# Kernel tuning notes

Hardware: AMD Instinct MI355X
Metric: run time of the kernel (lower is better)

The kernel has to match this reference:

```python
import jax, jax.numpy as jnp
import numpy as np

EMBED = 1024
HEADS = 16

def setup_inputs() -> dict:
    key = jax.random.key(0)
    k1, k2, k3, k4, k5 = jax.random.split(key, 5)
    x = jax.random.normal(k1, (2, 2048, EMBED), dtype=jnp.float32)
    s = 1.0 / np.sqrt(EMBED)
    W_atten = jax.random.normal(k2, (EMBED, 3 * EMBED), dtype=jnp.float32) * s
    b_atten = jax.random.normal(k3, (3 * EMBED,), dtype=jnp.float32) * 0.01
    W_proj = jax.random.normal(k4, (EMBED, EMBED), dtype=jnp.float32) * s
    b_proj = jax.random.normal(k5, (EMBED,), dtype=jnp.float32) * 0.01
    return {"x": x, "W_atten": W_atten, "b_atten": b_atten, "W_proj": W_proj, "b_proj": b_proj}

def reference(x, W_atten, b_atten, W_proj, b_proj):
    B, T, C = x.shape
    H = HEADS
    hs = C // H
    qkv = x @ W_atten + b_atten  # [B,T,3C]
    # NOTE: original splits as k, q, v (k first)
    k, q, v = jnp.split(qkv, 3, axis=2)
    k = k.reshape(B, T, H, hs).transpose(0, 2, 1, 3)  # [B,H,T,hs]
    q = q.reshape(B, T, H, hs).transpose(0, 2, 1, 3)
    v = v.reshape(B, T, H, hs).transpose(0, 2, 1, 3)
    scores = jnp.einsum('bhqd,bhkd->bhqk', q, k) / jnp.sqrt(jnp.float32(hs))
    causal = jnp.tril(jnp.ones((T, T), dtype=bool))
    scores = jnp.where(causal[None, None, :, :], scores, jnp.float32(-jnp.inf))
    att = jax.nn.softmax(scores, axis=-1)
    out = jnp.einsum('bhqk,bhkd->bhqd', att, v)  # [B,H,T,hs]
    out = out.transpose(0, 2, 1, 3).reshape(B, T, C)
    return out @ W_proj + b_proj
```

## Files before the change

kernel.cpp:

```cpp
#include <hip/hip_runtime.h>

typedef unsigned short u16;
typedef unsigned int u32;
typedef __bf16 bf16;
typedef bf16 bf16x8 __attribute__((ext_vector_type(8)));
typedef float f32x4 __attribute__((ext_vector_type(4)));
typedef u32 u32x4 __attribute__((ext_vector_type(4)));
typedef u16 u16x4 __attribute__((ext_vector_type(4)));

#define EMBED 1024
#define HEADS 16
#define HS 64
#define BATCH 2
#define SEQ 2048
#define M_TOT (BATCH * SEQ)
#define N_QKV (3 * EMBED)
#define KDIM  EMBED

#define CSCALE 0.18033688011112042f
#define MREF (64.0f * CSCALE)

__device__ __forceinline__ u16 f2bf(float f) {
  u32 u = __builtin_bit_cast(u32, f);
  u32 r = u + 0x7fffu + ((u >> 16) & 1u);
  return (u16)(r >> 16);
}
__device__ __forceinline__ float bf2f(u16 h) {
  return __builtin_bit_cast(float, (u32)h << 16);
}
__device__ __forceinline__ bf16x8 frag16(const u16* p) {
  return __builtin_bit_cast(bf16x8, *(const u32x4*)p);
}
__device__ __forceinline__ bf16x8 frag16u(const u32* p) {
  return __builtin_bit_cast(bf16x8, *(const u32x4*)p);
}
__device__ __forceinline__ float cl(float v) {
  return fminf(fmaxf(v, -3.0e4f), 3.0e4f);
}
__device__ __forceinline__ u32 pk2bf(float lo, float hi) {
  const u32 ul = __builtin_bit_cast(u32, lo) + 0x8000u;
  const u32 uh = __builtin_bit_cast(u32, hi) + 0x8000u;
  return (ul >> 16) | (uh & 0xFFFF0000u);
}

typedef __attribute__((address_space(1))) void gvoid;
typedef __attribute__((address_space(3))) void lvoid;
__device__ __forceinline__ void glds16(const u16* g, u16* l) {
  __builtin_amdgcn_global_load_lds((gvoid*)g, (lvoid*)l, 16, 0, 0);
}

__global__ __launch_bounds__(256) void convert_kernel(
    const float* __restrict__ in, u16* __restrict__ out, int n4) {
  const int i = blockIdx.x * 256 + threadIdx.x;
  if (i < n4) {
    f32x4 v = *(const f32x4*)(in + (size_t)i * 4);
    u16x4 pk;
#pragma unroll
    for (int j = 0; j < 4; j++) pk[j] = f2bf(v[j]);
    *(u16x4*)(out + (size_t)i * 4) = pk;
  }
}

__global__ __launch_bounds__(256) void transpose_conv_kernel(
    const float* __restrict__ in, u16* __restrict__ out, int R, int C) {
  __shared__ u16 tile[32][33];
  const int c0 = blockIdx.x * 32;
  const int r0 = blockIdx.y * 32;
  const int tx = threadIdx.x;
  const int ty = threadIdx.y;
#pragma unroll
  for (int i = 0; i < 32; i += 8)
    tile[ty + i][tx] = f2bf(in[(size_t)(r0 + ty + i) * C + c0 + tx]);
  __syncthreads();
#pragma unroll
  for (int i = 0; i < 32; i += 8)
    out[(size_t)(c0 + ty + i) * R + r0 + tx] = tile[tx][ty + i];
}

__global__ __launch_bounds__(256) void gemm_qkv_kernel(
    const u16* __restrict__ A, const u16* __restrict__ wt,
    const u16* __restrict__ bias, u16* __restrict__ kq, u16* __restrict__ vt) {
  __shared__ u16 As[128 * 32];
  __shared__ u16 Bs[128 * 32];
  const int tid = threadIdx.x;
  const int lane = tid & 63;
  const int wave = tid >> 6;
  const int quad = lane >> 4;
  const int l16 = lane & 15;
  const int wr = wave >> 1;
  const int wc = wave & 1;
  const int m0 = blockIdx.y * 128;
  const int n0 = blockIdx.x * 128;

  f32x4 acc[4][4] = {};
  const int grow = tid >> 2;
  const int gcol = (tid & 3) * 8;

  for (int k0 = 0; k0 < KDIM; k0 += 32) {
    __syncthreads();
    glds16(A + (size_t)(m0 + grow) * KDIM + k0 + gcol, As + tid * 8);
    glds16(A + (size_t)(m0 + grow + 64) * KDIM + k0 + gcol, As + 2048 + tid * 8);
    glds16(wt + (size_t)(n0 + grow) * KDIM + k0 + gcol, Bs + tid * 8);
    glds16(wt + (size_t)(n0 + grow + 64) * KDIM + k0 + gcol, Bs + 2048 + tid * 8);
    __syncthreads();

    bf16x8 af[4], bfr[4];
#pragma unroll
    for (int i = 0; i < 4; i++) {
      af[i]  = frag16(As + (wr * 64 + i * 16 + l16) * 32 + quad * 8);
      bfr[i] = frag16(Bs + (wc * 64 + i * 16 + l16) * 32 + quad * 8);
    }
#pragma unroll
    for (int mi = 0; mi < 4; mi++)
#pragma unroll
      for (int ni = 0; ni < 4; ni++)
        acc[mi][ni] = __builtin_amdgcn_mfma_f32_16x16x32_bf16(
            af[mi], bfr[ni], acc[mi][ni], 0, 0, 0);
  }

#pragma unroll
  for (int ni = 0; ni < 4; ni++) {
    const int n = n0 + wc * 64 + ni * 16 + l16;
    const float bv = bf2f(bias[n]);
    if (n < 2 * EMBED) {
#pragma unroll
      for (int mi = 0; mi < 4; mi++)
#pragma unroll
        for (int r = 0; r < 4; r++) {
          const int m = m0 + wr * 64 + mi * 16 + quad * 4 + r;
          kq[(size_t)m * 2048 + n] = f2bf(cl(acc[mi][ni][r] + bv));
        }
    } else {
      const int hd = n - 2 * EMBED;
      const int h2 = hd >> 6;
      const int dc2 = (hd >> 4) & 3;
#pragma unroll
      for (int mi = 0; mi < 4; mi++) {
        const int mbase = m0 + wr * 64 + mi * 16 + quad * 4;
        const int bqi = mbase >> 11;
        const int t0 = mbase & 2047;
        const int kt2 = t0 >> 6;
        const int kc2 = (t0 >> 5) & 1;
        const int qt2 = (t0 >> 3) & 3;
        const int e0 = t0 & 7;
        u16x4 pk;
#pragma unroll
        for (int r = 0; r < 4; r++) pk[r] = f2bf(cl(acc[mi][ni][r] + bv));
        const size_t idx =
            ((((size_t)(bqi * 16 + h2) * 32 + kt2) * 2 + kc2) * 4 + dc2) * 512 +
            (qt2 * 16 + l16) * 8 + e0;
        *(u16x4*)(vt + idx) = pk;
      }
    }
  }
}

__global__ __launch_bounds__(128) void gemm_proj_kernel(
    const u16* __restrict__ A, const u16* __restrict__ wt,
    const u16* __restrict__ bias, float* __restrict__ out) {
  __shared__ u16 As[128 * 32];
  __shared__ u16 Bs[64 * 32];
  const int tid = threadIdx.x;
  const int lane = tid & 63;
  const int wave = tid >> 6;
  const int quad = lane >> 4;
  const int l16 = lane & 15;
  const int m0 = blockIdx.y * 128;
  const int n0 = blockIdx.x * 64;

  f32x4 acc[4][4] = {};
  const int grow = tid >> 2;
  const int gcol = (tid & 3) * 8;

  for (int k0 = 0; k0 < KDIM; k0 += 32) {
    __syncthreads();
#pragma unroll
    for (int p = 0; p < 4; p++)
      glds16(A + (size_t)(m0 + p * 32 + grow) * KDIM + k0 + gcol,
             As + p * 1024 + tid * 8);
#pragma unroll
    for (int p = 0; p < 2; p++)
      glds16(wt + (size_t)(n0 + p * 32 + grow) * KDIM + k0 + gcol,
             Bs + p * 1024 + tid * 8);
    __syncthreads();

    bf16x8 af[4], bfr[4];
#pragma unroll
    for (int i = 0; i < 4; i++) {
      af[i]  = frag16(As + (wave * 64 + i * 16 + l16) * 32 + quad * 8);
      bfr[i] = frag16(Bs + (i * 16 + l16) * 32 + quad * 8);
    }
#pragma unroll
    for (int mi = 0; mi < 4; mi++)
#pragma unroll
      for (int ni = 0; ni < 4; ni++)
        acc[mi][ni] = __builtin_amdgcn_mfma_f32_16x16x32_bf16(
            af[mi], bfr[ni], acc[mi][ni], 0, 0, 0);
  }

#pragma unroll
  for (int ni = 0; ni < 4; ni++) {
    const int n = n0 + ni * 16 + l16;
    const float bv = bf2f(bias[n]);
#pragma unroll
    for (int mi = 0; mi < 4; mi++)
#pragma unroll
      for (int r = 0; r < 4; r++) {
        const int m = m0 + wave * 64 + mi * 16 + quad * 4 + r;
        out[(size_t)m * EMBED + n] = cl(acc[mi][ni][r] + bv);
      }
  }
}

__global__ __launch_bounds__(128) void attn_kernel(
    const u16* __restrict__ kq, const u16* __restrict__ vt,
    u16* __restrict__ att) {
  __shared__ u16 Ks[2][2][64 * 64];

  const int tid = threadIdx.x;
  const int lane = tid & 63;
  const int wave = tid >> 6;
  const int quad = (lane >> 4) & 3;
  const int l16 = lane & 15;
  const bool lohalf = (lane < 32);

  const int bh = blockIdx.x;
  const int yy = (int)blockIdx.y;
  const int qt32 = wave ? yy : (63 - yy);
  const int q0 = qt32 * 32;
  const int bq = bh >> 4;
  const int h = bh & 15;

  int qg[2];
  bf16x8 bq0[2], bq1[2];
#pragma unroll
  for (int g = 0; g < 2; g++) {
    qg[g] = q0 + g * 16 + l16;
    const size_t qrow = (size_t)(bq * SEQ + qg[g]) * 2048 + EMBED + h * HS;
    bq0[g] = frag16(kq + qrow + quad * 8);
    bq1[g] = frag16(kq + qrow + 32 + quad * 8);
  }

  const u16* kb = kq + (size_t)bq * SEQ * 2048 + h * HS;
  const u16* vb2 = vt + (size_t)(bq * 16 + h) * 32 * 4096;

  const int pi = ((l16 >> 2) & 1) * 8 + ((l16 >> 3) & 1) * 2 +
                 ((l16 >> 1) & 1) * 4 + (l16 & 1);
  const int psw = quad ^ (pi & 7);
  const int kap = (quad & 1) * 8 + ((quad >> 1) & 1) * 2;

  u32x4 onesu;
#pragma unroll
  for (int j = 0; j < 4; j++) onesu[j] = 0x3F803F80u;
  const bf16x8 ones8 = __builtin_bit_cast(bf16x8, onesu);

  f32x4 o[2][4] = {};
  f32x4 o4[2] = {};

  const int nkt = (qt32 >> 1) + 1;
  u16* ksw = (u16*)Ks[wave];

#pragma unroll
  for (int p = 0; p < 8; p++) {
    const int row = p * 8 + (lane >> 3);
    const int sgc = (lane & 7) ^ (row & 7);
    glds16(kb + (size_t)row * 2048 + sgc * 8, ksw + row * 64 + (lane & 7) * 8);
  }

  for (int kt = 0; kt < nkt; kt++) {
    const int k0 = kt * 64;
    asm volatile("s_waitcnt vmcnt(0)" ::: "memory");
    if (kt + 1 < nkt) {
      const int kn = k0 + 64;
      u16* dst = ksw + ((kt + 1) & 1) * (64 * 64);
#pragma unroll
      for (int p = 0; p < 8; p++) {
        const int row = p * 8 + (lane >> 3);
        const int sgc = (lane & 7) ^ (row & 7);
        glds16(kb + (size_t)(kn + row) * 2048 + sgc * 8, dst + row * 64 + (lane & 7) * 8);
      }
    }
    const u16* KsB = ksw + (kt & 1) * (64 * 64);

    bf16x8 va[2][4];
#pragma unroll
    for (int kc = 0; kc < 2; kc++)
#pragma unroll
      for (int dc = 0; dc < 4; dc++)
        va[kc][dc] = frag16(vb2 + (size_t)kt * 4096 +
                            ((kc * 4 + dc) * 64 + quad * 16 + l16) * 8);

    f32x4 st[2][4] = {};
    __builtin_amdgcn_s_setprio(1);
#pragma unroll
    for (int sub = 0; sub < 4; sub++) {
      const u16* kr = KsB + (sub * 16 + pi) * 64;
      const bf16x8 ka0 = frag16(kr + psw * 8);
      const bf16x8 ka1 = frag16(kr + (psw ^ 4) * 8);
#pragma unroll
      for (int g = 0; g < 2; g++) {
        st[g][sub] = __builtin_amdgcn_mfma_f32_16x16x32_bf16(
            ka0, bq0[g], st[g][sub], 0, 0, 0);
        st[g][sub] = __builtin_amdgcn_mfma_f32_16x16x32_bf16(
            ka1, bq1[g], st[g][sub], 0, 0, 0);
      }
    }
    __builtin_amdgcn_s_setprio(0);

    const bool diag = (kt == nkt - 1);
#pragma unroll
    for (int g = 0; g < 2; g++) {
      float p[4][4];
      if (diag) {
#pragma unroll
        for (int sub = 0; sub < 4; sub++)
#pragma unroll
          for (int r = 0; r < 4; r++) {
            const int key = k0 + sub * 16 + kap + (r >> 1) * 4 + (r & 1);
            const float e = __builtin_amdgcn_exp2f(st[g][sub][r] * CSCALE - MREF);
            p[sub][r] = (key <= qg[g]) ? e : 0.0f;
          }
      } else {
#pragma unroll
        for (int sub = 0; sub < 4; sub++)
#pragma unroll
          for (int r = 0; r < 4; r++)
            p[sub][r] = __builtin_amdgcn_exp2f(st[g][sub][r] * CSCALE - MREF);
      }

#pragma unroll
      for (int kc = 0; kc < 2; kc++) {
        const int s0 = kc * 2, s1 = kc * 2 + 1;
        const u32 An = pk2bf(p[s0][0], p[s0][1]);
        const u32 Bn = pk2bf(p[s1][0], p[s1][1]);
        const u32 Cn = pk2bf(p[s0][2], p[s0][3]);
        const u32 Dn = pk2bf(p[s1][2], p[s1][3]);
        const u32 V1 = __shfl_xor(lohalf ? Bn : An, 32);
        const u32 V2 = __shfl_xor(lohalf ? Dn : Cn, 32);
        u32x4 pr;
        pr[0] = lohalf ? An : V1;
        pr[1] = lohalf ? V1 : Bn;
        pr[2] = lohalf ? Cn : V2;
        pr[3] = lohalf ? V2 : Dn;
        const bf16x8 pb = __builtin_bit_cast(bf16x8, pr);

        __builtin_amdgcn_s_setprio(1);
#pragma unroll
        for (int dc = 0; dc < 4; dc++)
          o[g][dc] = __builtin_amdgcn_mfma_f32_16x16x32_bf16(
              va[kc][dc], pb, o[g][dc], 0, 0, 0);
        o4[g] = __builtin_amdgcn_mfma_f32_16x16x32_bf16(
            ones8, pb, o4[g], 0, 0, 0);
        __builtin_amdgcn_s_setprio(0);
      }
    }
  }

#pragma unroll
  for (int g = 0; g < 2; g++) {
    const float inv = 1.0f / o4[g][0];
    const size_t obase = (size_t)(bq * SEQ + qg[g]) * EMBED + h * HS;
#pragma unroll
    for (int dc = 0; dc < 4; dc++) {
      u16 sv[4];
#pragma unroll
      for (int r = 0; r < 4; r++) sv[r] = f2bf(cl(o[g][dc][r] * inv));
      *(u32*)(att + obase + dc * 16 + quad * 4) = (u32)sv[0] | ((u32)sv[1] << 16);
      *(u32*)(att + obase + dc * 16 + quad * 4 + 2) = (u32)sv[2] | ((u32)sv[3] << 16);
    }
  }
}

extern "C" void kernel_launch(void* const* d_in, const int* in_sizes, int n_in,
                              void* d_out, int out_size, void* d_ws,
                              size_t ws_size, hipStream_t stream) {
  const float* x       = (const float*)d_in[0];
  const float* W_atten = (const float*)d_in[1];
  const float* b_atten = (const float*)d_in[2];
  const float* W_proj  = (const float*)d_in[3];
  const float* b_proj  = (const float*)d_in[4];

  u16* wt_a = (u16*)d_ws;
  u16* wt_p = wt_a + (size_t)N_QKV * EMBED;
  u16* ba   = wt_p + (size_t)EMBED * EMBED;
  u16* bp   = ba + N_QKV;
  u16* xb   = bp + EMBED;
  u16* kq   = xb + (size_t)M_TOT * KDIM;
  u16* vt   = kq + (size_t)M_TOT * 2048;
  u16* attb = xb;

  convert_kernel<<<(M_TOT * KDIM / 4 + 255) / 256, 256, 0, stream>>>(
      x, xb, M_TOT * KDIM / 4);
  convert_kernel<<<(N_QKV / 4 + 255) / 256, 256, 0, stream>>>(b_atten, ba, N_QKV / 4);
  convert_kernel<<<(EMBED / 4 + 255) / 256, 256, 0, stream>>>(b_proj, bp, EMBED / 4);
  transpose_conv_kernel<<<dim3(N_QKV / 32, EMBED / 32), dim3(32, 8), 0, stream>>>(
      W_atten, wt_a, EMBED, N_QKV);
  transpose_conv_kernel<<<dim3(EMBED / 32, EMBED / 32), dim3(32, 8), 0, stream>>>(
      W_proj, wt_p, EMBED, EMBED);
  gemm_qkv_kernel<<<dim3(N_QKV / 128, M_TOT / 128), 256, 0, stream>>>(
      xb, wt_a, ba, kq, vt);
  attn_kernel<<<dim3(BATCH * HEADS, SEQ / 64), 128, 0, stream>>>(kq, vt, attb);
  gemm_proj_kernel<<<dim3(EMBED / 64, M_TOT / 128), 128, 0, stream>>>(
      attb, wt_p, bp, (float*)d_out);
}
```

Before: 193.3 us.

## Split each attention query tile's key range across two waves and merge via LDS

Previously each 128-thread block gave its two waves different 32-row query tiles, paired to balance causal work. Now both waves share one query tile and each processes half of its key tiles. Wave 1 writes its partial output accumulators and row sums to LDS, and wave 0 adds them before normalizing and storing. The grid's y dimension doubles so all query tiles are still covered. This shortens the per-wave serial loop and raises the number of blocks, at the cost of an LDS reduction, a barrier, and less even work per block since pairs are no longer balanced.

```diff
diff --git a/kernel.cpp b/kernel.cpp
--- a/kernel.cpp
+++ b/kernel.cpp
@@ -225,8 +225,7 @@
   const bool lohalf = (lane < 32);
 
   const int bh = blockIdx.x;
-  const int yy = (int)blockIdx.y;
-  const int qt32 = wave ? yy : (63 - yy);
+  const int qt32 = 63 - (int)blockIdx.y;
   const int q0 = qt32 * 32;
   const int bq = bh >> 4;
   const int h = bh & 15;
@@ -258,21 +257,27 @@
   f32x4 o4[2] = {};
 
   const int nkt = (qt32 >> 1) + 1;
+  const int half = nkt >> 1;
+  const int kstart = wave ? half : 0;
+  const int kend = wave ? nkt : half;
   u16* ksw = (u16*)Ks[wave];
 
-#pragma unroll
-  for (int p = 0; p < 8; p++) {
-    const int row = p * 8 + (lane >> 3);
-    const int sgc = (lane & 7) ^ (row & 7);
-    glds16(kb + (size_t)row * 2048 + sgc * 8, ksw + row * 64 + (lane & 7) * 8);
-  }
-
-  for (int kt = 0; kt < nkt; kt++) {
+  if (kstart < kend) {
+#pragma unroll
+    for (int p = 0; p < 8; p++) {
+      const int row = p * 8 + (lane >> 3);
+      const int sgc = (lane & 7) ^ (row & 7);
+      glds16(kb + (size_t)(kstart * 64 + row) * 2048 + sgc * 8,
+             ksw + (kstart & 1) * 4096 + row * 64 + (lane & 7) * 8);
+    }
+  }
+
+  for (int kt = kstart; kt < kend; kt++) {
     const int k0 = kt * 64;
     asm volatile("s_waitcnt vmcnt(0)" ::: "memory");
-    if (kt + 1 < nkt) {
+    if (kt + 1 < kend) {
       const int kn = k0 + 64;
-      u16* dst = ksw + ((kt + 1) & 1) * (64 * 64);
+      u16* dst = ksw + ((kt + 1) & 1) * 4096;
 #pragma unroll
       for (int p = 0; p < 8; p++) {
         const int row = p * 8 + (lane >> 3);
@@ -280,7 +285,7 @@
         glds16(kb + (size_t)(kn + row) * 2048 + sgc * 8, dst + row * 64 + (lane & 7) * 8);
       }
     }
-    const u16* KsB = ksw + (kt & 1) * (64 * 64);
+    const u16* KsB = ksw + (kt & 1) * 4096;
 
     bf16x8 va[2][4];
 #pragma unroll
@@ -356,17 +361,33 @@
     }
   }
 
-#pragma unroll
-  for (int g = 0; g < 2; g++) {
-    const float inv = 1.0f / o4[g][0];
-    const size_t obase = (size_t)(bq * SEQ + qg[g]) * EMBED + h * HS;
-#pragma unroll
-    for (int dc = 0; dc < 4; dc++) {
-      u16 sv[4];
-#pragma unroll
-      for (int r = 0; r < 4; r++) sv[r] = f2bf(cl(o[g][dc][r] * inv));
-      *(u32*)(att + obase + dc * 16 + quad * 4) = (u32)sv[0] | ((u32)sv[1] << 16);
-      *(u32*)(att + obase + dc * 16 + quad * 4 + 2) = (u32)sv[2] | ((u32)sv[3] << 16);
+  float* cb = (float*)Ks[1];
+  if (wave == 1) {
+#pragma unroll
+    for (int g = 0; g < 2; g++) {
+#pragma unroll
+      for (int dc = 0; dc < 4; dc++)
+        *(f32x4*)(cb + ((g * 4 + dc) * 64 + lane) * 4) = o[g][dc];
+      cb[2048 + g * 64 + lane] = o4[g][0];
+    }
+  }
+  __syncthreads();
+
+  if (wave == 0) {
+#pragma unroll
+    for (int g = 0; g < 2; g++) {
+      float lsum = o4[g][0] + cb[2048 + g * 64 + lane];
+      const float inv = 1.0f / lsum;
+      const size_t obase = (size_t)(bq * SEQ + qg[g]) * EMBED + h * HS;
+#pragma unroll
+      for (int dc = 0; dc < 4; dc++) {
+        const f32x4 ov = o[g][dc] + *(const f32x4*)(cb + ((g * 4 + dc) * 64 + lane) * 4);
+        u16 sv[4];
+#pragma unroll
+        for (int r = 0; r < 4; r++) sv[r] = f2bf(cl(ov[r] * inv));
+        *(u32*)(att + obase + dc * 16 + quad * 4) = (u32)sv[0] | ((u32)sv[1] << 16);
+        *(u32*)(att + obase + dc * 16 + quad * 4 + 2) = (u32)sv[2] | ((u32)sv[3] << 16);
+      }
     }
   }
 }
@@ -399,7 +420,7 @@
       W_proj, wt_p, EMBED, EMBED);
   gemm_qkv_kernel<<<dim3(N_QKV / 128, M_TOT / 128), 256, 0, stream>>>(
       xb, wt_a, ba, kq, vt);
-  attn_kernel<<<dim3(BATCH * HEADS, SEQ / 64), 128, 0, stream>>>(kq, vt, attb);
+  attn_kernel<<<dim3(BATCH * HEADS, SEQ / 32), 128, 0, stream>>>(kq, vt, attb);
   gemm_proj_kernel<<<dim3(EMBED / 64, M_TOT / 128), 128, 0, stream>>>(
       attb, wt_p, bp, (float*)d_out);
 }
```

Measured after the change: 184.8 us. -4.4%, faster.
